# Kernel optimization log

Hardware: AMD Instinct MI355X
Metric: run time of the kernel (lower is better)

The kernel has to match this reference:

```python
import jax, jax.numpy as jnp
import numpy as np


def _gcn(x, src, dst, W, b, n):
    # symmetric normalization: deg computed on edges WITH self-loops (weights 1)
    deg = jax.ops.segment_sum(jnp.ones_like(src, dtype=x.dtype), dst, num_segments=n)
    dinv = jnp.where(deg > 0, jax.lax.rsqrt(deg), 0.0)
    norm = dinv[src] * dinv[dst]              # [E+n]
    xw = x @ W                                # [n, out] transform first (cheaper)
    msg = xw[src] * norm[:, None]             # gather + edge scale
    return jax.ops.segment_sum(msg, dst, num_segments=n) + b


def setup_inputs() -> dict:
    key = jax.random.key(0)
    ks = jax.random.split(key, 8)
    N, E = 100_000, 1_280_000
    x = jax.random.normal(ks[0], (N, 18), dtype=jnp.float32)
    edge_index = jax.random.randint(ks[1], (2, E), 0, N, dtype=jnp.int32)
    W1 = jax.random.normal(ks[2], (18, 32), dtype=jnp.float32) * 0.2
    b1 = jnp.zeros((32,), dtype=jnp.float32)
    W2 = jax.random.normal(ks[3], (32, 64), dtype=jnp.float32) * 0.15
    b2 = jnp.zeros((64,), dtype=jnp.float32)
    Wfc = jax.random.normal(ks[4], (64, 2), dtype=jnp.float32) * 0.1
    bfc = jnp.zeros((2,), dtype=jnp.float32)
    return {"x": x, "edge_index": edge_index, "W1": W1, "b1": b1,
            "W2": W2, "b2": b2, "Wfc": Wfc, "bfc": bfc}


def reference(x, edge_index, W1, b1, W2, b2, Wfc, bfc):
    n = x.shape[0]
    loop = jnp.arange(n, dtype=edge_index.dtype)
    src = jnp.concatenate([edge_index[0], loop])   # add self-loops (PyG default)
    dst = jnp.concatenate([edge_index[1], loop])
    h = jax.nn.relu(_gcn(x, src, dst, W1, b1, n))
    h = jax.nn.relu(_gcn(h, src, dst, W2, b2, n))
    logits = h @ Wfc + bfc
    return jax.nn.log_softmax(logits, axis=1)
```

## Files before the change

### kernel.cpp

```cpp
#include <hip/hip_runtime.h>
#include <hip/hip_fp16.h>
#include <math.h>


#define TPB 256
#define BSH 8
#define BNODES 256
#define MAXBUCK 512
#define CH 8192
#define CAPSH 13
#define CAP (1 << CAPSH)

__global__ void k_part(const int* __restrict__ src, const int* __restrict__ dst,
                       int* __restrict__ bcursor, int* __restrict__ eb,
                       __half* __restrict__ u1h, __half* __restrict__ u2h,
                       int E, int n, int nbuck) {
    __shared__ int lh[MAXBUCK];
    __shared__ int lbase[MAXBUCK];
    int t = threadIdx.x;
    if (blockIdx.x == 0 && t < 32) {
        u1h[(size_t)n * 32 + t] = __float2half_rn(0.f);
        u2h[(size_t)n * 32 + t] = __float2half_rn(0.f);
    }
    int chunk0 = blockIdx.x * CH;
    int end = min(chunk0 + CH, E);
    const int4* dst4 = (const int4*)dst;
    const int4* src4 = (const int4*)src;
    for (int i = t; i < nbuck; i += TPB) lh[i] = 0;
    __syncthreads();
    for (int e4 = chunk0 / 4 + t; e4 * 4 < end; e4 += TPB) {
        int base = e4 * 4;
        int4 d = dst4[e4];
        if (base + 0 < end) atomicAdd(&lh[d.x >> BSH], 1);
        if (base + 1 < end) atomicAdd(&lh[d.y >> BSH], 1);
        if (base + 2 < end) atomicAdd(&lh[d.z >> BSH], 1);
        if (base + 3 < end) atomicAdd(&lh[d.w >> BSH], 1);
    }
    __syncthreads();
    for (int i = t; i < nbuck; i += TPB) {
        int c = lh[i];
        lbase[i] = c ? atomicAdd(&bcursor[i], c) : 0;
        lh[i] = 0;
    }
    __syncthreads();
    for (int e4 = chunk0 / 4 + t; e4 * 4 < end; e4 += TPB) {
        int base = e4 * 4;
        int4 d = dst4[e4];
        int4 s = src4[e4];
        #define PUT(c, sv) if (base + c < end) { \
            int b = (d.sv) >> BSH; \
            int r = lbase[b] + atomicAdd(&lh[b], 1); \
            if (r < CAP) \
                eb[((size_t)b << CAPSH) + r] = ((s.sv) << BSH) | ((d.sv) & (BNODES - 1)); }
        PUT(0, x) PUT(1, y) PUT(2, z) PUT(3, w)
        #undef PUT
    }
}

__global__ void k_bucket(const int* __restrict__ eb, const int* __restrict__ bcursor,
                         const float* __restrict__ x, const float* __restrict__ W1,
                         int* __restrict__ csr, int* __restrict__ row_start,
                         int* __restrict__ cnt8, float* __restrict__ dinv,
                         __half* __restrict__ u1h, int n) {
    __shared__ int lcnt[BNODES];
    __shared__ int lscan[BNODES];
    __shared__ float ldinv[BNODES];
    __shared__ float xs[BNODES * 18];
    int b = blockIdx.x;
    int t = threadIdx.x;
    int node0 = b << BSH;
    int beg = b << CAPSH;
    int end = beg + min(bcursor[b], CAP);
    lcnt[t] = 0;
    __syncthreads();
    for (int i = beg + t; i < end; i += TPB)
        atomicAdd(&lcnt[eb[i] & (BNODES - 1)], 1);
    __syncthreads();
    int v = lcnt[t];
    int pad = (v + 7) & ~7;
    lscan[t] = pad;
    __syncthreads();
    for (int off = 1; off < TPB; off <<= 1) {
        int xx = (t >= off) ? lscan[t - off] : 0;
        __syncthreads();
        lscan[t] += xx;
        __syncthreads();
    }
    int pexcl = lscan[t] - pad;
    int node = node0 + t;
    float dv = rsqrtf(1.0f + (float)v);
    ldinv[t] = dv;
    if (node < n) {
        row_start[node] = beg + pexcl;
        cnt8[node] = pad >> 3;
        dinv[node] = dv;
    }
    __syncthreads();
    lcnt[t] = pexcl;
    __syncthreads();
    for (int i = beg + t; i < end; i += TPB) {
        int e = eb[i];
        int p = atomicAdd(&lcnt[e & (BNODES - 1)], 1);
        csr[beg + p] = e >> BSH;
    }
    __syncthreads();
    for (int p = v; p < pad; ++p) csr[beg + pexcl + p] = n;
    int nn = min(BNODES, n - node0);
    const float* xb = x + (size_t)node0 * 18;
    int tot18 = nn * 18;
    for (int i = t; i < tot18; i += TPB) xs[i] = xb[i];
    __syncthreads();
    int f = t & 31, g = t >> 5;
    float w1r[18];
#pragma unroll
    for (int k = 0; k < 18; ++k) w1r[k] = W1[k * 32 + f];
    __half* ub = u1h + (size_t)node0 * 32;
    for (int nl = g; nl < nn; nl += 8) {
        const float* rp = &xs[nl * 18];
        float a = 0.f;
#pragma unroll
        for (int k = 0; k < 18; ++k) a = fmaf(rp[k], w1r[k], a);
        ub[nl * 32 + f] = __float2half_rn(a * ldinv[nl]);
    }
}

#define CVT4(vv, r0, r1, r2, r3) \
    { __half2* _p = (__half2*)&(vv); \
      float2 _fl = __half22float2(_p[0]), _fh = __half22float2(_p[1]); \
      r0 = _fl.x; r1 = _fl.y; r2 = _fh.x; r3 = _fh.y; }

#define GATHER8(uq, sA, sB, q, a0, a1, a2, a3) \
    { uint2 _v0 = uq[(size_t)(sA).x * 8 + (q)]; \
      uint2 _v1 = uq[(size_t)(sA).y * 8 + (q)]; \
      uint2 _v2 = uq[(size_t)(sA).z * 8 + (q)]; \
      uint2 _v3 = uq[(size_t)(sA).w * 8 + (q)]; \
      uint2 _v4 = uq[(size_t)(sB).x * 8 + (q)]; \
      uint2 _v5 = uq[(size_t)(sB).y * 8 + (q)]; \
      uint2 _v6 = uq[(size_t)(sB).z * 8 + (q)]; \
      uint2 _v7 = uq[(size_t)(sB).w * 8 + (q)]; \
      float _x0,_y0,_z0,_w0, _x1,_y1,_z1,_w1, _x2,_y2,_z2,_w2, _x3,_y3,_z3,_w3; \
      float _x4,_y4,_z4,_w4, _x5,_y5,_z5,_w5, _x6,_y6,_z6,_w6, _x7,_y7,_z7,_w7; \
      CVT4(_v0,_x0,_y0,_z0,_w0) CVT4(_v1,_x1,_y1,_z1,_w1) \
      CVT4(_v2,_x2,_y2,_z2,_w2) CVT4(_v3,_x3,_y3,_z3,_w3) \
      CVT4(_v4,_x4,_y4,_z4,_w4) CVT4(_v5,_x5,_y5,_z5,_w5) \
      CVT4(_v6,_x6,_y6,_z6,_w6) CVT4(_v7,_x7,_y7,_z7,_w7) \
      a0 += ((_x0+_x1)+(_x2+_x3)) + ((_x4+_x5)+(_x6+_x7)); \
      a1 += ((_y0+_y1)+(_y2+_y3)) + ((_y4+_y5)+(_y6+_y7)); \
      a2 += ((_z0+_z1)+(_z2+_z3)) + ((_z4+_z5)+(_z6+_z7)); \
      a3 += ((_w0+_w1)+(_w2+_w3)) + ((_w4+_w5)+(_w6+_w7)); }

__global__ void k_fused1(const uint2* __restrict__ u1q, const int* __restrict__ row_start,
                         const int* __restrict__ cnt8, const int* __restrict__ csr,
                         const float* __restrict__ dinv,
                         const float* __restrict__ b1, __half* __restrict__ u2h,
                         int n) {
    int t = threadIdx.x;
    int lane = t & 63, wv = t >> 6;
    int q = lane & 7, grp = lane >> 3;
    int node = (blockIdx.x * 4 + wv) * 8 + grp;
    if (node >= n) return;
    float4 bb = ((const float4*)b1)[q];
    uint2 sv = u1q[(size_t)node * 8 + q];
    float a0, a1, a2, a3;
    CVT4(sv, a0, a1, a2, a3)
    int beg = row_start[node];
    int it = cnt8[node];
    const int4* ip = (const int4*)(csr + beg);
    if (it > 0) {
        int4 sA = ip[0], sB = ip[1];
        for (int i = 0; i < it; ++i) {
            int4 nA = ip[2 * i + 2];
            int4 nB = ip[2 * i + 3];
            GATHER8(u1q, sA, sB, q, a0, a1, a2, a3)
            sA = nA; sB = nB;
        }
    }
    float di = dinv[node];
    float r0 = fmaxf(fmaf(di, a0, bb.x), 0.f) * di;
    float r1 = fmaxf(fmaf(di, a1, bb.y), 0.f) * di;
    float r2 = fmaxf(fmaf(di, a2, bb.z), 0.f) * di;
    float r3 = fmaxf(fmaf(di, a3, bb.w), 0.f) * di;
    uint2 st;
    __half2* sp = (__half2*)&st;
    sp[0].x = __float2half_rn(r0); sp[0].y = __float2half_rn(r1);
    sp[1].x = __float2half_rn(r2); sp[1].y = __float2half_rn(r3);
    ((uint2*)u2h)[(size_t)node * 8 + q] = st;
}

__global__ void k_fused2(const uint2* __restrict__ u2q, const int* __restrict__ row_start,
                         const int* __restrict__ cnt8, const int* __restrict__ csr,
                         const float* __restrict__ dinv,
                         const float* __restrict__ W2,
                         const float* __restrict__ b2, const float* __restrict__ Wfc,
                         const float* __restrict__ bfc, float* __restrict__ out,
                         int n) {
    __shared__ float lagg[4][8][33];
    int t = threadIdx.x;
    int lane = t & 63, wv = t >> 6;
    int q = lane & 7, grp = lane >> 3;
    float w2r[32];
#pragma unroll
    for (int k = 0; k < 32; ++k) w2r[k] = W2[k * 64 + lane];
    float b2v = b2[lane];
    float wf0 = Wfc[lane * 2 + 0], wf1 = Wfc[lane * 2 + 1];
    float bf0 = bfc[0], bf1 = bfc[1];
    int node0 = (blockIdx.x * 4 + wv) * 8;
    int node = node0 + grp;
    float a0 = 0.f, a1 = 0.f, a2 = 0.f, a3 = 0.f;
    if (node < n) {
        uint2 sv = u2q[(size_t)node * 8 + q];
        float s0, s1, s2, s3;
        CVT4(sv, s0, s1, s2, s3)
        a0 = s0; a1 = s1; a2 = s2; a3 = s3;
        int beg = row_start[node];
        int it = cnt8[node];
        const int4* ip = (const int4*)(csr + beg);
        if (it > 0) {
            int4 sA = ip[0], sB = ip[1];
            for (int i = 0; i < it; ++i) {
                int4 nA = ip[2 * i + 2];
                int4 nB = ip[2 * i + 3];
                GATHER8(u2q, sA, sB, q, a0, a1, a2, a3)
                sA = nA; sB = nB;
            }
        }
    }
    lagg[wv][grp][4 * q + 0] = a0;
    lagg[wv][grp][4 * q + 1] = a1;
    lagg[wv][grp][4 * q + 2] = a2;
    lagg[wv][grp][4 * q + 3] = a3;
#pragma unroll
    for (int r = 0; r < 8; ++r) {
        int nodeT = node0 + r;
        const float* rp = lagg[wv][r];
        float c0 = 0.f, c1 = 0.f, c2 = 0.f, c3 = 0.f;
#pragma unroll
        for (int k = 0; k < 32; k += 4) {
            c0 = fmaf(rp[k],     w2r[k],     c0);
            c1 = fmaf(rp[k + 1], w2r[k + 1], c1);
            c2 = fmaf(rp[k + 2], w2r[k + 2], c2);
            c3 = fmaf(rp[k + 3], w2r[k + 3], c3);
        }
        float a = (c0 + c1) + (c2 + c3);
        float v = (nodeT < n) ? fmaxf(fmaf(dinv[nodeT], a, b2v), 0.f) : 0.f;
        float l0 = v * wf0;
        float l1 = v * wf1;
#pragma unroll
        for (int off = 32; off >= 1; off >>= 1) {
            l0 += __shfl_xor(l0, off, 64);
            l1 += __shfl_xor(l1, off, 64);
        }
        if (lane == 0 && nodeT < n) {
            l0 += bf0;
            l1 += bf1;
            float m2 = fmaxf(l0, l1);
            float lse = m2 + logf(expf(l0 - m2) + expf(l1 - m2));
            out[nodeT * 2 + 0] = l0 - lse;
            out[nodeT * 2 + 1] = l1 - lse;
        }
    }
}

extern "C" void kernel_launch(void* const* d_in, const int* in_sizes, int n_in,
                              void* d_out, int out_size, void* d_ws, size_t ws_size,
                              hipStream_t stream) {
    const float* x   = (const float*)d_in[0];
    const int*   ei  = (const int*)d_in[1];
    const float* W1  = (const float*)d_in[2];
    const float* b1  = (const float*)d_in[3];
    const float* W2  = (const float*)d_in[4];
    const float* b2  = (const float*)d_in[5];
    const float* Wfc = (const float*)d_in[6];
    const float* bfc = (const float*)d_in[7];
    float* out = (float*)d_out;

    const int n = in_sizes[0] / 18;
    const int E = in_sizes[1] / 2;
    const int* src = ei;
    const int* dst = ei + E;
    const int nbuck = (n + BNODES - 1) >> BSH;

    char* w = (char*)d_ws;
    int*    bcursor   = (int*)w;     w += (size_t)nbuck * 4;
    int*    row_start = (int*)w;     w += (size_t)n * 4;
    int*    cnt8      = (int*)w;     w += (size_t)n * 4;
    float*  dinv      = (float*)w;   w += (size_t)n * 4;
    int*    eb        = (int*)w;     w += (size_t)nbuck * CAP * 4;
    int*    csr       = (int*)w;     w += (size_t)nbuck * CAP * 4 + 64;
    w = (char*)(((size_t)w + 63) & ~(size_t)63);
    __half* u1h       = (__half*)w;  w += (size_t)(n + 1) * 32 * 2;
    w = (char*)(((size_t)w + 63) & ~(size_t)63);
    __half* u2h       = (__half*)w;  w += (size_t)(n + 1) * 32 * 2;

    hipMemsetAsync(bcursor, 0, (size_t)nbuck * 4, stream);
    k_part<<<(E + CH - 1) / CH, TPB, 0, stream>>>(src, dst, bcursor, eb, u1h, u2h, E, n, nbuck);
    k_bucket<<<nbuck, TPB, 0, stream>>>(eb, bcursor, x, W1, csr, row_start, cnt8,
                                        dinv, u1h, n);

    const int waves = (n + 7) / 8;
    const int blocksF = (waves + 3) / 4;

    k_fused1<<<blocksF, TPB, 0, stream>>>((const uint2*)u1h, row_start, cnt8, csr,
                                          dinv, b1, u2h, n);
    k_fused2<<<blocksF, TPB, 0, stream>>>((const uint2*)u2h, row_start, cnt8, csr,
                                          dinv, W2, b2, Wfc, bfc, out, n);
}
```

Before: 172.3 us.

## Stage partitioned edges in shared memory for coalesced writes; add gathered rows in half2

The edge partition kernel now computes a block-local exclusive scan of bucket counts and places each edge into a bucket-sorted shared-memory staging buffer. It then writes the staged edges to the global bucket arrays in contiguous runs, replacing scattered per-edge stores. The chunk size is halved so the staging buffer fits in LDS. Separately, the gather loops in both aggregation kernels add the eight neighbour rows with packed half2 adds before converting to float, which cuts conversion and FP32 add work but loses some accumulation precision.

```diff
diff --git a/kernel.cpp b/kernel.cpp
--- a/kernel.cpp
+++ b/kernel.cpp
@@ -7,7 +7,7 @@
 #define BSH 8
 #define BNODES 256
 #define MAXBUCK 512
-#define CH 8192
+#define CH 4096
 #define CAPSH 13
 #define CAP (1 << CAPSH)
 
@@ -16,7 +16,10 @@
                        __half* __restrict__ u1h, __half* __restrict__ u2h,
                        int E, int n, int nbuck) {
     __shared__ int lh[MAXBUCK];
+    __shared__ int lexc[MAXBUCK];
     __shared__ int lbase[MAXBUCK];
+    __shared__ int sval[CH];
+    __shared__ unsigned short sbk[CH];
     int t = threadIdx.x;
     if (blockIdx.x == 0 && t < 32) {
         u1h[(size_t)n * 32 + t] = __float2half_rn(0.f);
@@ -24,9 +27,10 @@
     }
     int chunk0 = blockIdx.x * CH;
     int end = min(chunk0 + CH, E);
+    int cnt = end - chunk0;
     const int4* dst4 = (const int4*)dst;
     const int4* src4 = (const int4*)src;
-    for (int i = t; i < nbuck; i += TPB) lh[i] = 0;
+    for (int i = t; i < MAXBUCK; i += TPB) lh[i] = 0;
     __syncthreads();
     for (int e4 = chunk0 / 4 + t; e4 * 4 < end; e4 += TPB) {
         int base = e4 * 4;
@@ -37,9 +41,21 @@
         if (base + 3 < end) atomicAdd(&lh[d.w >> BSH], 1);
     }
     __syncthreads();
-    for (int i = t; i < nbuck; i += TPB) {
+    for (int i = t; i < MAXBUCK; i += TPB) lexc[i] = lh[i];
+    __syncthreads();
+    for (int off = 1; off < MAXBUCK; off <<= 1) {
+        int i1 = t + TPB;
+        int v0 = (t >= off) ? lexc[t - off] : 0;
+        int v1 = (i1 >= off) ? lexc[i1 - off] : 0;
+        __syncthreads();
+        lexc[t] += v0;
+        lexc[i1] += v1;
+        __syncthreads();
+    }
+    for (int i = t; i < MAXBUCK; i += TPB) {
         int c = lh[i];
         lbase[i] = c ? atomicAdd(&bcursor[i], c) : 0;
+        lexc[i] -= c;
         lh[i] = 0;
     }
     __syncthreads();
@@ -47,13 +63,19 @@
         int base = e4 * 4;
         int4 d = dst4[e4];
         int4 s = src4[e4];
-        #define PUT(c, sv) if (base + c < end) { \
+        #define PUTL(c, sv) if (base + c < end) { \
             int b = (d.sv) >> BSH; \
-            int r = lbase[b] + atomicAdd(&lh[b], 1); \
-            if (r < CAP) \
-                eb[((size_t)b << CAPSH) + r] = ((s.sv) << BSH) | ((d.sv) & (BNODES - 1)); }
-        PUT(0, x) PUT(1, y) PUT(2, z) PUT(3, w)
-        #undef PUT
+            int p = lexc[b] + atomicAdd(&lh[b], 1); \
+            sval[p] = ((s.sv) << BSH) | ((d.sv) & (BNODES - 1)); \
+            sbk[p] = (unsigned short)b; }
+        PUTL(0, x) PUTL(1, y) PUTL(2, z) PUTL(3, w)
+        #undef PUTL
+    }
+    __syncthreads();
+    for (int i = t; i < cnt; i += TPB) {
+        int b = sbk[i];
+        int r = lbase[b] + (i - lexc[b]);
+        if (r < CAP) eb[((size_t)b << CAPSH) + r] = sval[i];
     }
 }
 
@@ -129,7 +151,7 @@
       float2 _fl = __half22float2(_p[0]), _fh = __half22float2(_p[1]); \
       r0 = _fl.x; r1 = _fl.y; r2 = _fh.x; r3 = _fh.y; }
 
-#define GATHER8(uq, sA, sB, q, a0, a1, a2, a3) \
+#define GATHER8H(uq, sA, sB, q, a0, a1, a2, a3) \
     { uint2 _v0 = uq[(size_t)(sA).x * 8 + (q)]; \
       uint2 _v1 = uq[(size_t)(sA).y * 8 + (q)]; \
       uint2 _v2 = uq[(size_t)(sA).z * 8 + (q)]; \
@@ -138,16 +160,22 @@
       uint2 _v5 = uq[(size_t)(sB).y * 8 + (q)]; \
       uint2 _v6 = uq[(size_t)(sB).z * 8 + (q)]; \
       uint2 _v7 = uq[(size_t)(sB).w * 8 + (q)]; \
-      float _x0,_y0,_z0,_w0, _x1,_y1,_z1,_w1, _x2,_y2,_z2,_w2, _x3,_y3,_z3,_w3; \
-      float _x4,_y4,_z4,_w4, _x5,_y5,_z5,_w5, _x6,_y6,_z6,_w6, _x7,_y7,_z7,_w7; \
-      CVT4(_v0,_x0,_y0,_z0,_w0) CVT4(_v1,_x1,_y1,_z1,_w1) \
-      CVT4(_v2,_x2,_y2,_z2,_w2) CVT4(_v3,_x3,_y3,_z3,_w3) \
-      CVT4(_v4,_x4,_y4,_z4,_w4) CVT4(_v5,_x5,_y5,_z5,_w5) \
-      CVT4(_v6,_x6,_y6,_z6,_w6) CVT4(_v7,_x7,_y7,_z7,_w7) \
-      a0 += ((_x0+_x1)+(_x2+_x3)) + ((_x4+_x5)+(_x6+_x7)); \
-      a1 += ((_y0+_y1)+(_y2+_y3)) + ((_y4+_y5)+(_y6+_y7)); \
-      a2 += ((_z0+_z1)+(_z2+_z3)) + ((_z4+_z5)+(_z6+_z7)); \
-      a3 += ((_w0+_w1)+(_w2+_w3)) + ((_w4+_w5)+(_w6+_w7)); }
+      __half2* _h0 = (__half2*)&_v0; __half2* _h1 = (__half2*)&_v1; \
+      __half2* _h2 = (__half2*)&_v2; __half2* _h3 = (__half2*)&_v3; \
+      __half2* _h4 = (__half2*)&_v4; __half2* _h5 = (__half2*)&_v5; \
+      __half2* _h6 = (__half2*)&_v6; __half2* _h7 = (__half2*)&_v7; \
+      __half2 _A01 = __hadd2(_h0[0], _h1[0]), _A23 = __hadd2(_h2[0], _h3[0]); \
+      __half2 _A45 = __hadd2(_h4[0], _h5[0]), _A67 = __hadd2(_h6[0], _h7[0]); \
+      __half2 _B01 = __hadd2(_h0[1], _h1[1]), _B23 = __hadd2(_h2[1], _h3[1]); \
+      __half2 _B45 = __hadd2(_h4[1], _h5[1]), _B67 = __hadd2(_h6[1], _h7[1]); \
+      __half2 _A03 = __hadd2(_A01, _A23), _A47 = __hadd2(_A45, _A67); \
+      __half2 _B03 = __hadd2(_B01, _B23), _B47 = __hadd2(_B45, _B67); \
+      float2 _fa0 = __half22float2(_A03), _fa1 = __half22float2(_A47); \
+      float2 _fb0 = __half22float2(_B03), _fb1 = __half22float2(_B47); \
+      a0 += _fa0.x + _fa1.x; \
+      a1 += _fa0.y + _fa1.y; \
+      a2 += _fb0.x + _fb1.x; \
+      a3 += _fb0.y + _fb1.y; }
 
 __global__ void k_fused1(const uint2* __restrict__ u1q, const int* __restrict__ row_start,
                          const int* __restrict__ cnt8, const int* __restrict__ csr,
@@ -171,7 +199,7 @@
         for (int i = 0; i < it; ++i) {
             int4 nA = ip[2 * i + 2];
             int4 nB = ip[2 * i + 3];
-            GATHER8(u1q, sA, sB, q, a0, a1, a2, a3)
+            GATHER8H(u1q, sA, sB, q, a0, a1, a2, a3)
             sA = nA; sB = nB;
         }
     }
@@ -220,7 +248,7 @@
             for (int i = 0; i < it; ++i) {
                 int4 nA = ip[2 * i + 2];
                 int4 nB = ip[2 * i + 3];
-                GATHER8(u2q, sA, sB, q, a0, a1, a2, a3)
+                GATHER8H(u2q, sA, sB, q, a0, a1, a2, a3)
                 sA = nA; sB = nB;
             }
         }
```

Measured after the change: 170.1 us. Within noise of the previous version (-1.2%).
